# Optimization experiments

Hardware: AMD Instinct MI355X
Metric: run time of the kernel (lower is better)

Reference implementation:

```python
import jax, jax.numpy as jnp
import numpy as np

D, H, L, FF = 512, 8, 6, 2048
EPS = 1e-5


def _ln(x, g, b):
    m = x.mean(-1, keepdims=True)
    v = ((x - m) ** 2).mean(-1, keepdims=True)
    return (x - m) * jax.lax.rsqrt(v + EPS) * g + b


def _mha(qi, ki, vi, w, b):
    # w: [4, D, D] (q, k, v, out), b: [4, D]; weights stored [in, out]
    B, Sq, _ = qi.shape
    Sk = ki.shape[1]
    dk = D // H
    q = (qi @ w[0] + b[0]).reshape(B, Sq, H, dk)
    k = (ki @ w[1] + b[1]).reshape(B, Sk, H, dk)
    v = (vi @ w[2] + b[2]).reshape(B, Sk, H, dk)
    scores = jnp.einsum('bqhd,bkhd->bhqk', q, k) / np.float32(np.sqrt(dk))
    attn = jax.nn.softmax(scores, axis=-1)
    o = jnp.einsum('bhqk,bkhd->bqhd', attn, v).reshape(B, Sq, D)
    return o @ w[3] + b[3]


def setup_inputs() -> dict:
    key = jax.random.key(0)
    ks = jax.random.split(key, 12)
    bs, c, h, w = 4, D, 32, 32
    nq = 100
    s = np.float32(0.02)
    f32 = jnp.float32
    return {
        'src': jax.random.normal(ks[0], (bs, c, h, w), f32),
        'query_embed': jax.random.normal(ks[1], (nq, D), f32),
        'pos_embed': jax.random.normal(ks[2], (bs, c, h, w), f32),
        # encoder params (stacked over L layers)
        'enc_attn_w': jax.random.normal(ks[3], (L, 4, D, D), f32) * s,
        'enc_attn_b': jnp.zeros((L, 4, D), f32),
        'enc_w1': jax.random.normal(ks[4], (L, D, FF), f32) * s,
        'enc_b1': jnp.zeros((L, FF), f32),
        'enc_w2': jax.random.normal(ks[5], (L, FF, D), f32) * s,
        'enc_b2': jnp.zeros((L, D), f32),
        'enc_ln_w': jnp.ones((L, 2, D), f32),
        'enc_ln_b': jnp.zeros((L, 2, D), f32),
        # decoder params
        'dec_sa_w': jax.random.normal(ks[6], (L, 4, D, D), f32) * s,
        'dec_sa_b': jnp.zeros((L, 4, D), f32),
        'dec_ca_w': jax.random.normal(ks[7], (L, 4, D, D), f32) * s,
        'dec_ca_b': jnp.zeros((L, 4, D), f32),
        'dec_w1': jax.random.normal(ks[8], (L, D, FF), f32) * s,
        'dec_b1': jnp.zeros((L, FF), f32),
        'dec_w2': jax.random.normal(ks[9], (L, FF, D), f32) * s,
        'dec_b2': jnp.zeros((L, D), f32),
        'dec_ln_w': jnp.ones((L, 3, D), f32),
        'dec_ln_b': jnp.zeros((L, 3, D), f32),
    }


def reference(src, query_embed, pos_embed,
              enc_attn_w, enc_attn_b, enc_w1, enc_b1, enc_w2, enc_b2,
              enc_ln_w, enc_ln_b,
              dec_sa_w, dec_sa_b, dec_ca_w, dec_ca_b,
              dec_w1, dec_b1, dec_w2, dec_b2, dec_ln_w, dec_ln_b):
    bs, c, h, w = src.shape
    x = src.reshape(bs, c, h * w).transpose(0, 2, 1)        # [B, HW, D]
    pos = pos_embed.reshape(bs, c, h * w).transpose(0, 2, 1)  # [B, HW, D]
    qe = jnp.broadcast_to(query_embed[None], (bs,) + query_embed.shape)  # [B, NQ, D]

    def enc_step(mem, p):
        aw, ab, w1, b1, w2, b2, lnw, lnb = p
        t = mem + pos  # original re-adds pos_embed every encoder layer
        t = _ln(t + _mha(t, t, t, aw, ab), lnw[0], lnb[0])
        f = jax.nn.relu(t @ w1 + b1) @ w2 + b2
        t = _ln(t + f, lnw[1], lnb[1])
        return t, None

    memory, _ = jax.lax.scan(
        enc_step, x,
        (enc_attn_w, enc_attn_b, enc_w1, enc_b1, enc_w2, enc_b2, enc_ln_w, enc_ln_b))

    mem_in = memory + pos

    def dec_step(out, p):
        saw, sab, caw, cab, w1, b1, w2, b2, lnw, lnb = p
        t = out + qe  # original re-adds query_embed every decoder layer
        t = _ln(t + _mha(t, t, t, saw, sab), lnw[0], lnb[0])
        t = _ln(t + _mha(t, mem_in, mem_in, caw, cab), lnw[1], lnb[1])
        f = jax.nn.relu(t @ w1 + b1) @ w2 + b2
        t = _ln(t + f, lnw[2], lnb[2])
        return t, None

    tgt = jnp.zeros_like(qe)
    output, _ = jax.lax.scan(
        dec_step, tgt,
        (dec_sa_w, dec_sa_b, dec_ca_w, dec_ca_b, dec_w1, dec_b1, dec_w2, dec_b2,
         dec_ln_w, dec_ln_b))
    return output, memory
```

## Files before the change

kernel.cpp:

```cpp
#include <hip/hip_runtime.h>
#include <math.h>


typedef unsigned short bfu;
typedef unsigned int u32;
typedef __bf16 bf8v __attribute__((ext_vector_type(8)));
typedef float f32x4 __attribute__((ext_vector_type(4)));

__device__ inline bfu f2bf(float f) {
  union { float f; u32 u; } v; v.f = f;
  u32 u = v.u;
  u32 r = (u + 0x7fffu + ((u >> 16) & 1u)) >> 16;
  return (bfu)r;
}
__device__ inline float bflo(u32 u) { return __uint_as_float(u << 16); }

typedef const __attribute__((address_space(1))) u32 gas_t;
typedef __attribute__((address_space(3))) u32 las_t;
__device__ __forceinline__ void gl16(const void* g, void* l) {
  __builtin_amdgcn_global_load_lds((gas_t*)g, (las_t*)l, 16, 0, 0);
}

__global__ __launch_bounds__(256) void k_transpose(const float* __restrict__ in,
                                                   float* __restrict__ out) {
  __shared__ float tile[32][33];
  int b = blockIdx.z;
  int c0 = blockIdx.x * 32, s0 = blockIdx.y * 32;
  int tx = threadIdx.x, ty = threadIdx.y;
  for (int i = ty; i < 32; i += 8)
    tile[i][tx] = in[((size_t)(b * 512 + c0 + i)) * 1024 + s0 + tx];
  __syncthreads();
  for (int i = ty; i < 32; i += 8)
    out[((size_t)(b * 1024 + s0 + i)) * 512 + c0 + tx] = tile[tx][i];
}

__global__ __launch_bounds__(256) void k_wt(const float* __restrict__ src,
                                            bfu* __restrict__ dst,
                                            int K, int N, int nj, int lstride) {
  __shared__ bfu tile[32][33];
  int g = blockIdx.z;
  int l = g / nj, j = g - l * nj;
  const float* s = src + ((size_t)l * lstride + j) * (size_t)K * N;
  bfu* d = dst + (size_t)g * (size_t)K * N;
  int n0 = blockIdx.x * 32, k0 = blockIdx.y * 32;
  int tx = threadIdx.x, ty = threadIdx.y;
  for (int i = ty; i < 32; i += 8)
    tile[i][tx] = f2bf(s[(size_t)(k0 + i) * N + n0 + tx]);
  __syncthreads();
  for (int i = ty; i < 32; i += 8)
    d[(size_t)(n0 + i) * K + k0 + tx] = tile[tx][i];
}

__global__ void k_add_dual(const float* __restrict__ a, const float* __restrict__ b,
                           float* __restrict__ of, bfu* __restrict__ ob, int n4) {
  int i = blockIdx.x * blockDim.x + threadIdx.x;
  if (i >= n4) return;
  float4 x = ((const float4*)a)[i];
  float4 y = ((const float4*)b)[i];
  float4 r = make_float4(x.x + y.x, x.y + y.y, x.z + y.z, x.w + y.w);
  if (of) ((float4*)of)[i] = r;
  if (ob) ((ushort4*)ob)[i] = make_ushort4(f2bf(r.x), f2bf(r.y), f2bf(r.z), f2bf(r.w));
}

__global__ void k_add_qe_dual(const float* __restrict__ a, const float* __restrict__ qe,
                              float* __restrict__ of, bfu* __restrict__ ob) {
  int i = blockIdx.x * blockDim.x + threadIdx.x;
  if (i >= 51200) return;
  int row = i >> 7;
  int q = row % 100;
  int c4 = i & 127;
  float4 x = ((const float4*)a)[i];
  float4 y = ((const float4*)qe)[q * 128 + c4];
  float4 r = make_float4(x.x + y.x, x.y + y.y, x.z + y.z, x.w + y.w);
  if (of) ((float4*)of)[i] = r;
  if (ob) ((ushort4*)ob)[i] = make_ushort4(f2bf(r.x), f2bf(r.y), f2bf(r.z), f2bf(r.w));
}

__global__ void k_zero(float* __restrict__ o, int n4) {
  int i = blockIdx.x * blockDim.x + threadIdx.x;
  if (i < n4) ((float4*)o)[i] = make_float4(0.f, 0.f, 0.f, 0.f);
}

__global__ __launch_bounds__(256) void k_ln_red(const float* __restrict__ A,
                                                const float* __restrict__ P,
                                                int nsplit, size_t pz,
                                                const float* __restrict__ bias,
                                                const float* __restrict__ g,
                                                const float* __restrict__ be,
                                                float* __restrict__ of,
                                                bfu* __restrict__ ob, int rows) {
  int row = blockIdx.x * 4 + (threadIdx.x >> 6);
  int lane = threadIdx.x & 63;
  if (row >= rows) return;
  const float* pa = A + (size_t)row * 512;
  float v[8];
  float s = 0.f, s2 = 0.f;
#pragma unroll
  for (int j = 0; j < 8; ++j) {
    int c = lane + j * 64;
    float x = pa[c] + bias[c];
    for (int z = 0; z < nsplit; ++z) x += P[z * pz + (size_t)row * 512 + c];
    v[j] = x; s += x; s2 += x * x;
  }
#pragma unroll
  for (int off = 32; off > 0; off >>= 1) {
    s += __shfl_xor(s, off);
    s2 += __shfl_xor(s2, off);
  }
  float mean = s * (1.f / 512.f);
  float var = s2 * (1.f / 512.f) - mean * mean;
  float r = rsqrtf(var + 1e-5f);
#pragma unroll
  for (int j = 0; j < 8; ++j) {
    int c = lane + j * 64;
    float o = (v[j] - mean) * r * g[c] + be[c];
    of[(size_t)row * 512 + c] = o;
    if (ob) ob[(size_t)row * 512 + c] = f2bf(o);
  }
}

__global__ __launch_bounds__(256) void k_gemm_bf(const bfu* __restrict__ A,
                                                 const bfu* __restrict__ Wt,
                                                 const float* __restrict__ bias,
                                                 bfu* __restrict__ C,
                                                 int M, int N, int K, int relu,
                                                 size_t wtz, size_t cz, int bz) {
  __shared__ bfu As[2][128][64];
  __shared__ bfu Bs[2][128][64];
  int z = blockIdx.z;
  Wt += (size_t)z * wtz; C += (size_t)z * cz; bias += z * bz;
  int bm = blockIdx.y * 128, bn = blockIdx.x * 128;
  int t = threadIdx.x;
  int wave = t >> 6, lane = t & 63;
  int wm = wave >> 1, wn = wave & 1;
  int l15 = lane & 15, l4 = lane >> 4;
  f32x4 acc[4][4];
  f32x4 zz = {0.f, 0.f, 0.f, 0.f};
#pragma unroll
  for (int mi = 0; mi < 4; ++mi)
#pragma unroll
    for (int ni = 0; ni < 4; ++ni) acc[mi][ni] = zz;

  auto stage = [&](int buf, int k0) {
#pragma unroll
    for (int i = 0; i < 4; ++i) {
      int c = t + i * 256;
      int row = c >> 3, kg = c & 7;
      int sc = kg ^ (row & 7);
      if (bm + row < M)
        gl16(A + (size_t)(bm + row) * K + k0 + sc * 8, &As[buf][row][kg * 8]);
      gl16(Wt + (size_t)(bn + row) * K + k0 + sc * 8, &Bs[buf][row][kg * 8]);
    }
  };
  stage(0, 0);
  int cur = 0;
  for (int k0 = 0; k0 < K; k0 += 64) {
    __syncthreads();
    if (k0 + 64 < K) stage(cur ^ 1, k0 + 64);
#pragma unroll
    for (int kc = 0; kc < 2; ++kc) {
      bf8v av[4], bv[4];
#pragma unroll
      for (int mi = 0; mi < 4; ++mi) {
        int row = wm * 64 + mi * 16 + l15;
        av[mi] = *(const bf8v*)&As[cur][row][((kc * 4 + l4) ^ (row & 7)) * 8];
      }
#pragma unroll
      for (int ni = 0; ni < 4; ++ni) {
        int row = wn * 64 + ni * 16 + l15;
        bv[ni] = *(const bf8v*)&Bs[cur][row][((kc * 4 + l4) ^ (row & 7)) * 8];
      }
#pragma unroll
      for (int mi = 0; mi < 4; ++mi)
#pragma unroll
        for (int ni = 0; ni < 4; ++ni)
          acc[mi][ni] = __builtin_amdgcn_mfma_f32_16x16x32_bf16(av[mi], bv[ni],
                                                                acc[mi][ni], 0, 0, 0);
    }
    cur ^= 1;
  }

#pragma unroll
  for (int mi = 0; mi < 4; ++mi) {
    int row0 = bm + wm * 64 + mi * 16 + l4 * 4;
#pragma unroll
    for (int ni = 0; ni < 4; ++ni) {
      int col = bn + wn * 64 + ni * 16 + l15;
      float bb = bias[col];
#pragma unroll
      for (int r = 0; r < 4; ++r) {
        int row = row0 + r;
        if (row < M) {
          float v = acc[mi][ni][r] + bb;
          if (relu) v = fmaxf(v, 0.f);
          C[(size_t)row * N + col] = f2bf(v);
        }
      }
    }
  }
}

__global__ __launch_bounds__(256) void k_gemm_sk(const bfu* __restrict__ A,
                                                 const bfu* __restrict__ Wt,
                                                 float* __restrict__ Pf,
                                                 int M, int N, int K, int ksplit) {
  __shared__ bfu As[2][128][64];
  __shared__ bfu Bs[2][128][64];
  int z = blockIdx.z;
  int Kc = K / ksplit;
  int kbeg = z * Kc;
  Pf += (size_t)z * M * N;
  int bm = blockIdx.y * 128, bn = blockIdx.x * 128;
  int t = threadIdx.x;
  int wave = t >> 6, lane = t & 63;
  int wm = wave >> 1, wn = wave & 1;
  int l15 = lane & 15, l4 = lane >> 4;
  f32x4 acc[4][4];
  f32x4 zz = {0.f, 0.f, 0.f, 0.f};
#pragma unroll
  for (int mi = 0; mi < 4; ++mi)
#pragma unroll
    for (int ni = 0; ni < 4; ++ni) acc[mi][ni] = zz;

  auto stage = [&](int buf, int k0) {
#pragma unroll
    for (int i = 0; i < 4; ++i) {
      int c = t + i * 256;
      int row = c >> 3, kg = c & 7;
      int sc = kg ^ (row & 7);
      if (bm + row < M)
        gl16(A + (size_t)(bm + row) * K + k0 + sc * 8, &As[buf][row][kg * 8]);
      gl16(Wt + (size_t)(bn + row) * K + k0 + sc * 8, &Bs[buf][row][kg * 8]);
    }
  };
  stage(0, kbeg);
  int cur = 0;
  for (int k0 = kbeg; k0 < kbeg + Kc; k0 += 64) {
    __syncthreads();
    if (k0 + 64 < kbeg + Kc) stage(cur ^ 1, k0 + 64);
#pragma unroll
    for (int kc = 0; kc < 2; ++kc) {
      bf8v av[4], bv[4];
#pragma unroll
      for (int mi = 0; mi < 4; ++mi) {
        int row = wm * 64 + mi * 16 + l15;
        av[mi] = *(const bf8v*)&As[cur][row][((kc * 4 + l4) ^ (row & 7)) * 8];
      }
#pragma unroll
      for (int ni = 0; ni < 4; ++ni) {
        int row = wn * 64 + ni * 16 + l15;
        bv[ni] = *(const bf8v*)&Bs[cur][row][((kc * 4 + l4) ^ (row & 7)) * 8];
      }
#pragma unroll
      for (int mi = 0; mi < 4; ++mi)
#pragma unroll
        for (int ni = 0; ni < 4; ++ni)
          acc[mi][ni] = __builtin_amdgcn_mfma_f32_16x16x32_bf16(av[mi], bv[ni],
                                                                acc[mi][ni], 0, 0, 0);
    }
    cur ^= 1;
  }

#pragma unroll
  for (int mi = 0; mi < 4; ++mi) {
    int row0 = bm + wm * 64 + mi * 16 + l4 * 4;
#pragma unroll
    for (int ni = 0; ni < 4; ++ni) {
      int col = bn + wn * 64 + ni * 16 + l15;
#pragma unroll
      for (int r = 0; r < 4; ++r) {
        int row = row0 + r;
        if (row < M) Pf[(size_t)row * N + col] = acc[mi][ni][r];
      }
    }
  }
}

__global__ __launch_bounds__(256) void k_attn_mfma(const bfu* __restrict__ Q, int qs,
                                                   const bfu* __restrict__ Km,
                                                   const bfu* __restrict__ Vm, int kvs,
                                                   bfu* __restrict__ O,
                                                   int Sq, int Sk) {
  __shared__ bfu Ks[64][72];
  __shared__ bfu Vt[64][72];
  __shared__ bfu Sm[4][16][72];
  const float scale = 0.125f;
  int b = blockIdx.z, h = blockIdx.y;
  int q0 = blockIdx.x * 64;
  int t = threadIdx.x;
  int wave = t >> 6, lane = t & 63;
  int l15 = lane & 15, l4 = lane >> 4;
  int hoff = h * 64;

  uint4 uq0 = {0u, 0u, 0u, 0u}, uq1 = {0u, 0u, 0u, 0u};
  {
    int qrow = q0 + wave * 16 + l15;
    if (qrow < Sq) {
      const bfu* qp = Q + (size_t)(b * Sq + qrow) * qs + hoff + l4 * 8;
      uq0 = *(const uint4*)qp;
      uq1 = *(const uint4*)(qp + 32);
    }
  }
  bf8v qf0 = *(bf8v*)&uq0, qf1 = *(bf8v*)&uq1;

  float m_[4] = {-1e30f, -1e30f, -1e30f, -1e30f};
  float l_[4] = {0.f, 0.f, 0.f, 0.f};
  f32x4 oacc[4];
  f32x4 zz = {0.f, 0.f, 0.f, 0.f};
#pragma unroll
  for (int n = 0; n < 4; ++n) oacc[n] = zz;

  uint4 ruk[2], ruv[2];
  const uint4 uz = {0u, 0u, 0u, 0u};
  auto load_kv = [&](int k0) {
#pragma unroll
    for (int i = 0; i < 2; ++i) {
      int e = t + i * 256;
      int rk = e >> 3, cg = e & 7;
      ruk[i] = uz;
      if (k0 + rk < Sk)
        ruk[i] = *(const uint4*)(Km + (size_t)(b * Sk + k0 + rk) * kvs + hoff + cg * 8);
      int kv = e & 63, dg = e >> 6;
      ruv[i] = uz;
      if (k0 + kv < Sk)
        ruv[i] = *(const uint4*)(Vm + (size_t)(b * Sk + k0 + kv) * kvs + hoff + dg * 8);
    }
  };
  load_kv(0);

  for (int k0 = 0; k0 < Sk; k0 += 64) {
#pragma unroll
    for (int i = 0; i < 2; ++i) {
      int e = t + i * 256;
      int rk = e >> 3, cg = e & 7;
      *(uint4*)&Ks[rk][cg * 8] = ruk[i];
      int kv = e & 63, dg = e >> 6;
      bfu vv[8];
      *(uint4*)vv = ruv[i];
#pragma unroll
      for (int j = 0; j < 8; ++j) Vt[dg * 8 + j][kv] = vv[j];
    }
    __syncthreads();
    if (k0 + 64 < Sk) load_kv(k0 + 64);

    f32x4 s4[4];
#pragma unroll
    for (int tt = 0; tt < 4; ++tt) {
      bf8v kf0 = *(const bf8v*)&Ks[tt * 16 + l15][l4 * 8];
      bf8v kf1 = *(const bf8v*)&Ks[tt * 16 + l15][32 + l4 * 8];
      f32x4 a = zz;
      a = __builtin_amdgcn_mfma_f32_16x16x32_bf16(qf0, kf0, a, 0, 0, 0);
      a = __builtin_amdgcn_mfma_f32_16x16x32_bf16(qf1, kf1, a, 0, 0, 0);
      s4[tt] = a;
    }

    float f_[4];
#pragma unroll
    for (int r = 0; r < 4; ++r) {
      float sv[4];
      float mx = -1e30f;
#pragma unroll
      for (int tt = 0; tt < 4; ++tt) {
        float s = s4[tt][r] * scale;
        s = (k0 + tt * 16 + l15 < Sk) ? s : -1e30f;
        sv[tt] = s;
        mx = fmaxf(mx, s);
      }
#pragma unroll
      for (int off = 1; off < 16; off <<= 1) mx = fmaxf(mx, __shfl_xor(mx, off));
      float nm = fmaxf(m_[r], mx);
      float f = __expf(m_[r] - nm);
      float ps = 0.f;
#pragma unroll
      for (int tt = 0; tt < 4; ++tt) {
        float p = __expf(sv[tt] - nm);
        ps += p;
        Sm[wave][l4 * 4 + r][tt * 16 + l15] = f2bf(p);
      }
#pragma unroll
      for (int off = 1; off < 16; off <<= 1) ps += __shfl_xor(ps, off);
      l_[r] = l_[r] * f + ps;
      m_[r] = nm;
      f_[r] = f;
    }
#pragma unroll
    for (int n = 0; n < 4; ++n)
#pragma unroll
      for (int r = 0; r < 4; ++r) oacc[n][r] *= f_[r];

    bf8v p0 = *(const bf8v*)&Sm[wave][l15][l4 * 8];
    bf8v p1 = *(const bf8v*)&Sm[wave][l15][32 + l4 * 8];
#pragma unroll
    for (int n = 0; n < 4; ++n) {
      bf8v v0 = *(const bf8v*)&Vt[n * 16 + l15][l4 * 8];
      bf8v v1 = *(const bf8v*)&Vt[n * 16 + l15][32 + l4 * 8];
      oacc[n] = __builtin_amdgcn_mfma_f32_16x16x32_bf16(p0, v0, oacc[n], 0, 0, 0);
      oacc[n] = __builtin_amdgcn_mfma_f32_16x16x32_bf16(p1, v1, oacc[n], 0, 0, 0);
    }
    __syncthreads();
  }

#pragma unroll
  for (int r = 0; r < 4; ++r) {
    int row = q0 + wave * 16 + l4 * 4 + r;
    if (row < Sq) {
      float inv = 1.f / l_[r];
#pragma unroll
      for (int n = 0; n < 4; ++n)
        O[(size_t)(b * Sq + row) * 512 + hoff + n * 16 + l15] = f2bf(oacc[n][r] * inv);
    }
  }
}


extern "C" void kernel_launch(void* const* d_in, const int* in_sizes, int n_in,
                              void* d_out, int out_size, void* d_ws, size_t ws_size,
                              hipStream_t stream) {
  const float* src         = (const float*)d_in[0];
  const float* query_embed = (const float*)d_in[1];
  const float* pos_embed   = (const float*)d_in[2];
  const float* enc_attn_w  = (const float*)d_in[3];
  const float* enc_attn_b  = (const float*)d_in[4];
  const float* enc_w1      = (const float*)d_in[5];
  const float* enc_b1      = (const float*)d_in[6];
  const float* enc_w2      = (const float*)d_in[7];
  const float* enc_b2      = (const float*)d_in[8];
  const float* enc_ln_w    = (const float*)d_in[9];
  const float* enc_ln_b    = (const float*)d_in[10];
  const float* dec_sa_w    = (const float*)d_in[11];
  const float* dec_sa_b    = (const float*)d_in[12];
  const float* dec_ca_w    = (const float*)d_in[13];
  const float* dec_ca_b    = (const float*)d_in[14];
  const float* dec_w1      = (const float*)d_in[15];
  const float* dec_b1      = (const float*)d_in[16];
  const float* dec_w2      = (const float*)d_in[17];
  const float* dec_b2      = (const float*)d_in[18];
  const float* dec_ln_w    = (const float*)d_in[19];
  const float* dec_ln_b    = (const float*)d_in[20];
  float* out = (float*)d_out;

  const size_t ENC = 4UL * 1024 * 512;
  const size_t DEC = 4UL * 100 * 512;
  const size_t MAT = 512UL * 512;

  float* p = (float*)d_ws;
  float* x    = p; p += ENC;
  float* pos  = p; p += ENC;
  float* t1   = p; p += ENC;
  float* t2   = p; p += ENC;
  float* t3   = p; p += DEC;
  float* dstr = p; p += DEC;
  float* Pf   = p; p += 4 * ENC;

  bfu* bp = (bfu*)p;
  bfu* t1b    = bp; bp += ENC;
  bfu* t2b    = bp; bp += ENC;
  bfu* t3b    = bp; bp += DEC;
  bfu* qkvb   = bp; bp += 4096UL * 1536;
  bfu* aob    = bp; bp += ENC;
  bfu* mob    = bp; bp += ENC;
  bfu* hbb    = bp; bp += 4096UL * 2048;
  bfu* meminb = bp; bp += ENC;
  bfu* ckvb   = bp; bp += 6UL * 4096 * 1024;
  bfu* enc_qkv_t = bp; bp += 18 * MAT;
  bfu* enc_out_t = bp; bp += 6 * MAT;
  bfu* enc_w1t   = bp; bp += 6UL * 512 * 2048;
  bfu* enc_w2t   = bp; bp += 6UL * 2048 * 512;
  bfu* dsa_qkv_t = bp; bp += 18 * MAT;
  bfu* dsa_out_t = bp; bp += 6 * MAT;
  bfu* dca_q_t   = bp; bp += 6 * MAT;
  bfu* dca_kv_t  = bp; bp += 12 * MAT;
  bfu* dca_out_t = bp; bp += 6 * MAT;
  bfu* dw1t      = bp; bp += 6UL * 512 * 2048;
  bfu* dw2t      = bp; bp += 6UL * 2048 * 512;

  dim3 tb(32, 8);
  k_transpose<<<dim3(16, 32, 4), tb, 0, stream>>>(src, x);
  k_transpose<<<dim3(16, 32, 4), tb, 0, stream>>>(pos_embed, pos);

  k_wt<<<dim3(16, 16, 18), tb, 0, stream>>>(enc_attn_w,            enc_qkv_t, 512, 512, 3, 4);
  k_wt<<<dim3(16, 16, 6),  tb, 0, stream>>>(enc_attn_w + 3 * MAT,  enc_out_t, 512, 512, 1, 4);
  k_wt<<<dim3(64, 16, 6),  tb, 0, stream>>>(enc_w1,                enc_w1t,   512, 2048, 1, 1);
  k_wt<<<dim3(16, 64, 6),  tb, 0, stream>>>(enc_w2,                enc_w2t,   2048, 512, 1, 1);
  k_wt<<<dim3(16, 16, 18), tb, 0, stream>>>(dec_sa_w,              dsa_qkv_t, 512, 512, 3, 4);
  k_wt<<<dim3(16, 16, 6),  tb, 0, stream>>>(dec_sa_w + 3 * MAT,    dsa_out_t, 512, 512, 1, 4);
  k_wt<<<dim3(16, 16, 6),  tb, 0, stream>>>(dec_ca_w,              dca_q_t,   512, 512, 1, 4);
  k_wt<<<dim3(16, 16, 12), tb, 0, stream>>>(dec_ca_w + 1 * MAT,    dca_kv_t,  512, 512, 2, 4);
  k_wt<<<dim3(16, 16, 6),  tb, 0, stream>>>(dec_ca_w + 3 * MAT,    dca_out_t, 512, 512, 1, 4);
  k_wt<<<dim3(64, 16, 6),  tb, 0, stream>>>(dec_w1,                dw1t,      512, 2048, 1, 1);
  k_wt<<<dim3(16, 64, 6),  tb, 0, stream>>>(dec_w2,                dw2t,      2048, 512, 1, 1);

  for (int l = 0; l < 6; ++l) {
    const float* ab = enc_attn_b + (size_t)l * 2048;
    float* xout = (l == 5) ? (out + DEC) : x;
    k_add_dual<<<2048, 256, 0, stream>>>(x, pos, t1, t1b, (int)(ENC / 4));
    k_gemm_bf<<<dim3(12, 32), 256, 0, stream>>>(t1b, enc_qkv_t + (size_t)l * 3 * MAT, ab,
                                                qkvb, 4096, 1536, 512, 0, 0, 0, 0);
    k_attn_mfma<<<dim3(16, 8, 4), 256, 0, stream>>>(qkvb, 1536, qkvb + 512, qkvb + 1024, 1536,
                                                    aob, 1024, 1024);
    k_gemm_sk<<<dim3(4, 32, 2), 256, 0, stream>>>(aob, enc_out_t + (size_t)l * MAT, Pf,
                                                  4096, 512, 512, 2);
    k_ln_red<<<1024, 256, 0, stream>>>(t1, Pf, 2, ENC, ab + 1536,
                                       enc_ln_w + (size_t)(l * 2 + 0) * 512,
                                       enc_ln_b + (size_t)(l * 2 + 0) * 512, t2, t2b, 4096);
    k_gemm_bf<<<dim3(16, 32), 256, 0, stream>>>(t2b, enc_w1t + (size_t)l * 512 * 2048,
                                                enc_b1 + (size_t)l * 2048, hbb,
                                                4096, 2048, 512, 1, 0, 0, 0);
    k_gemm_sk<<<dim3(4, 32, 4), 256, 0, stream>>>(hbb, enc_w2t + (size_t)l * 2048 * 512, Pf,
                                                  4096, 512, 2048, 4);
    k_ln_red<<<1024, 256, 0, stream>>>(t2, Pf, 4, ENC, enc_b2 + (size_t)l * 512,
                                       enc_ln_w + (size_t)(l * 2 + 1) * 512,
                                       enc_ln_b + (size_t)(l * 2 + 1) * 512,
                                       xout, (bfu*)nullptr, 4096);
  }

  k_add_dual<<<2048, 256, 0, stream>>>(out + DEC, pos, (float*)nullptr, meminb, (int)(ENC / 4));
  k_zero<<<200, 256, 0, stream>>>(dstr, (int)(DEC / 4));

  k_gemm_bf<<<dim3(8, 32, 6), 256, 0, stream>>>(meminb, dca_kv_t, dec_ca_b + 512,
                                                ckvb, 4096, 1024, 512, 0,
                                                2 * MAT, 4096UL * 1024, 2048);

  for (int l = 0; l < 6; ++l) {
    const float* sb = dec_sa_b + (size_t)l * 2048;
    const float* cb = dec_ca_b + (size_t)l * 2048;
    float* dout = (l == 5) ? out : dstr;
    k_add_qe_dual<<<200, 256, 0, stream>>>(dstr, query_embed, t1, t1b);
    k_gemm_bf<<<dim3(12, 4), 256, 0, stream>>>(t1b, dsa_qkv_t + (size_t)l * 3 * MAT, sb,
                                               qkvb, 400, 1536, 512, 0, 0, 0, 0);
    k_attn_mfma<<<dim3(2, 8, 4), 256, 0, stream>>>(qkvb, 1536, qkvb + 512, qkvb + 1024, 1536,
                                                   aob, 100, 100);
    k_gemm_sk<<<dim3(4, 4, 2), 256, 0, stream>>>(aob, dsa_out_t + (size_t)l * MAT, Pf,
                                                 400, 512, 512, 2);
    k_ln_red<<<100, 256, 0, stream>>>(t1, Pf, 2, 400UL * 512, sb + 1536,
                                      dec_ln_w + (size_t)(l * 3 + 0) * 512,
                                      dec_ln_b + (size_t)(l * 3 + 0) * 512, t2, t2b, 400);
    k_gemm_bf<<<dim3(4, 4), 256, 0, stream>>>(t2b, dca_q_t + (size_t)l * MAT, cb,
                                              qkvb, 400, 512, 512, 0, 0, 0, 0);
    k_attn_mfma<<<dim3(2, 8, 4), 256, 0, stream>>>(qkvb, 512,
                                                   ckvb + (size_t)l * 4096 * 1024,
                                                   ckvb + (size_t)l * 4096 * 1024 + 512, 1024,
                                                   aob, 100, 1024);
    k_gemm_sk<<<dim3(4, 4, 2), 256, 0, stream>>>(aob, dca_out_t + (size_t)l * MAT, Pf,
                                                 400, 512, 512, 2);
    k_ln_red<<<100, 256, 0, stream>>>(t2, Pf, 2, 400UL * 512, cb + 1536,
                                      dec_ln_w + (size_t)(l * 3 + 1) * 512,
                                      dec_ln_b + (size_t)(l * 3 + 1) * 512, t3, t3b, 400);
    k_gemm_bf<<<dim3(16, 4), 256, 0, stream>>>(t3b, dw1t + (size_t)l * 512 * 2048,
                                               dec_b1 + (size_t)l * 2048, hbb,
                                               400, 2048, 512, 1, 0, 0, 0);
    k_gemm_sk<<<dim3(4, 4, 4), 256, 0, stream>>>(hbb, dw2t + (size_t)l * 2048 * 512, Pf,
                                                 400, 512, 2048, 4);
    k_ln_red<<<100, 256, 0, stream>>>(t3, Pf, 4, 400UL * 512, dec_b2 + (size_t)l * 512,
                                      dec_ln_w + (size_t)(l * 3 + 2) * 512,
                                      dec_ln_b + (size_t)(l * 3 + 2) * 512,
                                      dout, (bfu*)nullptr, 400);
  }
}
```

Baseline: 2.034 ms.

## Fuse positional/query embedding adds into LayerNorm epilogue and widen attention KV tiles

The final LayerNorm of each encoder/decoder layer now also adds pos_embed (or query_embed) and writes the next layer's fp32 and bf16 inputs. This removes the separate add kernels, the zeroing kernel and the extra tensor round-trips. The attention kernel also processes 128 keys per tile instead of 64 and raises wave priority around the MFMA sections, halving loop iterations and barriers. The cost is more LDS and registers per block, which may reduce occupancy.

```diff
diff --git a/kernel.cpp b/kernel.cpp
--- a/kernel.cpp
+++ b/kernel.cpp
@@ -58,27 +58,20 @@
   float4 x = ((const float4*)a)[i];
   float4 y = ((const float4*)b)[i];
   float4 r = make_float4(x.x + y.x, x.y + y.y, x.z + y.z, x.w + y.w);
-  if (of) ((float4*)of)[i] = r;
-  if (ob) ((ushort4*)ob)[i] = make_ushort4(f2bf(r.x), f2bf(r.y), f2bf(r.z), f2bf(r.w));
-}
-
-__global__ void k_add_qe_dual(const float* __restrict__ a, const float* __restrict__ qe,
-                              float* __restrict__ of, bfu* __restrict__ ob) {
+  ((float4*)of)[i] = r;
+  ((ushort4*)ob)[i] = make_ushort4(f2bf(r.x), f2bf(r.y), f2bf(r.z), f2bf(r.w));
+}
+
+__global__ void k_qe0(const float* __restrict__ qe, float* __restrict__ of,
+                      bfu* __restrict__ ob) {
   int i = blockIdx.x * blockDim.x + threadIdx.x;
   if (i >= 51200) return;
   int row = i >> 7;
   int q = row % 100;
   int c4 = i & 127;
-  float4 x = ((const float4*)a)[i];
   float4 y = ((const float4*)qe)[q * 128 + c4];
-  float4 r = make_float4(x.x + y.x, x.y + y.y, x.z + y.z, x.w + y.w);
-  if (of) ((float4*)of)[i] = r;
-  if (ob) ((ushort4*)ob)[i] = make_ushort4(f2bf(r.x), f2bf(r.y), f2bf(r.z), f2bf(r.w));
-}
-
-__global__ void k_zero(float* __restrict__ o, int n4) {
-  int i = blockIdx.x * blockDim.x + threadIdx.x;
-  if (i < n4) ((float4*)o)[i] = make_float4(0.f, 0.f, 0.f, 0.f);
+  ((float4*)of)[i] = y;
+  ((ushort4*)ob)[i] = make_ushort4(f2bf(y.x), f2bf(y.y), f2bf(y.z), f2bf(y.w));
 }
 
 __global__ __launch_bounds__(256) void k_ln_red(const float* __restrict__ A,
@@ -88,7 +81,12 @@
                                                 const float* __restrict__ g,
                                                 const float* __restrict__ be,
                                                 float* __restrict__ of,
-                                                bfu* __restrict__ ob, int rows) {
+                                                bfu* __restrict__ ob,
+                                                const float* __restrict__ add2,
+                                                int qe_mode,
+                                                float* __restrict__ of2,
+                                                bfu* __restrict__ ob2,
+                                                int rows) {
   int row = blockIdx.x * 4 + (threadIdx.x >> 6);
   int lane = threadIdx.x & 63;
   if (row >= rows) return;
@@ -110,12 +108,18 @@
   float mean = s * (1.f / 512.f);
   float var = s2 * (1.f / 512.f) - mean * mean;
   float r = rsqrtf(var + 1e-5f);
+  int arow = qe_mode ? (row % 100) : row;
 #pragma unroll
   for (int j = 0; j < 8; ++j) {
     int c = lane + j * 64;
     float o = (v[j] - mean) * r * g[c] + be[c];
-    of[(size_t)row * 512 + c] = o;
+    if (of) of[(size_t)row * 512 + c] = o;
     if (ob) ob[(size_t)row * 512 + c] = f2bf(o);
+    if (add2) {
+      float o2 = o + add2[(size_t)arow * 512 + c];
+      if (of2) of2[(size_t)row * 512 + c] = o2;
+      if (ob2) ob2[(size_t)row * 512 + c] = f2bf(o2);
+    }
   }
 }
 
@@ -281,9 +285,9 @@
                                                    const bfu* __restrict__ Vm, int kvs,
                                                    bfu* __restrict__ O,
                                                    int Sq, int Sk) {
-  __shared__ bfu Ks[64][72];
-  __shared__ bfu Vt[64][72];
-  __shared__ bfu Sm[4][16][72];
+  __shared__ bfu Ks[128][72];
+  __shared__ bfu Vt[64][136];
+  __shared__ bfu Sm[4][16][136];
   const float scale = 0.125f;
   int b = blockIdx.z, h = blockIdx.y;
   int q0 = blockIdx.x * 64;
@@ -310,17 +314,17 @@
 #pragma unroll
   for (int n = 0; n < 4; ++n) oacc[n] = zz;
 
-  uint4 ruk[2], ruv[2];
+  uint4 ruk[4], ruv[4];
   const uint4 uz = {0u, 0u, 0u, 0u};
   auto load_kv = [&](int k0) {
 #pragma unroll
-    for (int i = 0; i < 2; ++i) {
+    for (int i = 0; i < 4; ++i) {
       int e = t + i * 256;
       int rk = e >> 3, cg = e & 7;
       ruk[i] = uz;
       if (k0 + rk < Sk)
         ruk[i] = *(const uint4*)(Km + (size_t)(b * Sk + k0 + rk) * kvs + hoff + cg * 8);
-      int kv = e & 63, dg = e >> 6;
+      int kv = e & 127, dg = e >> 7;
       ruv[i] = uz;
       if (k0 + kv < Sk)
         ruv[i] = *(const uint4*)(Vm + (size_t)(b * Sk + k0 + kv) * kvs + hoff + dg * 8);
@@ -328,24 +332,25 @@
   };
   load_kv(0);
 
-  for (int k0 = 0; k0 < Sk; k0 += 64) {
-#pragma unroll
-    for (int i = 0; i < 2; ++i) {
+  for (int k0 = 0; k0 < Sk; k0 += 128) {
+#pragma unroll
+    for (int i = 0; i < 4; ++i) {
       int e = t + i * 256;
       int rk = e >> 3, cg = e & 7;
       *(uint4*)&Ks[rk][cg * 8] = ruk[i];
-      int kv = e & 63, dg = e >> 6;
+      int kv = e & 127, dg = e >> 7;
       bfu vv[8];
       *(uint4*)vv = ruv[i];
 #pragma unroll
       for (int j = 0; j < 8; ++j) Vt[dg * 8 + j][kv] = vv[j];
     }
     __syncthreads();
-    if (k0 + 64 < Sk) load_kv(k0 + 64);
-
-    f32x4 s4[4];
-#pragma unroll
-    for (int tt = 0; tt < 4; ++tt) {
+    if (k0 + 128 < Sk) load_kv(k0 + 128);
+
+    f32x4 s4[8];
+    __builtin_amdgcn_s_setprio(1);
+#pragma unroll
+    for (int tt = 0; tt < 8; ++tt) {
       bf8v kf0 = *(const bf8v*)&Ks[tt * 16 + l15][l4 * 8];
       bf8v kf1 = *(const bf8v*)&Ks[tt * 16 + l15][32 + l4 * 8];
       f32x4 a = zz;
@@ -353,14 +358,15 @@
       a = __builtin_amdgcn_mfma_f32_16x16x32_bf16(qf1, kf1, a, 0, 0, 0);
       s4[tt] = a;
     }
+    __builtin_amdgcn_s_setprio(0);
 
     float f_[4];
 #pragma unroll
     for (int r = 0; r < 4; ++r) {
-      float sv[4];
+      float sv[8];
       float mx = -1e30f;
 #pragma unroll
-      for (int tt = 0; tt < 4; ++tt) {
+      for (int tt = 0; tt < 8; ++tt) {
         float s = s4[tt][r] * scale;
         s = (k0 + tt * 16 + l15 < Sk) ? s : -1e30f;
         sv[tt] = s;
@@ -372,7 +378,7 @@
       float f = __expf(m_[r] - nm);
       float ps = 0.f;
 #pragma unroll
-      for (int tt = 0; tt < 4; ++tt) {
+      for (int tt = 0; tt < 8; ++tt) {
         float p = __expf(sv[tt] - nm);
         ps += p;
         Sm[wave][l4 * 4 + r][tt * 16 + l15] = f2bf(p);
@@ -388,15 +394,20 @@
 #pragma unroll
       for (int r = 0; r < 4; ++r) oacc[n][r] *= f_[r];
 
-    bf8v p0 = *(const bf8v*)&Sm[wave][l15][l4 * 8];
-    bf8v p1 = *(const bf8v*)&Sm[wave][l15][32 + l4 * 8];
-#pragma unroll
-    for (int n = 0; n < 4; ++n) {
-      bf8v v0 = *(const bf8v*)&Vt[n * 16 + l15][l4 * 8];
-      bf8v v1 = *(const bf8v*)&Vt[n * 16 + l15][32 + l4 * 8];
-      oacc[n] = __builtin_amdgcn_mfma_f32_16x16x32_bf16(p0, v0, oacc[n], 0, 0, 0);
-      oacc[n] = __builtin_amdgcn_mfma_f32_16x16x32_bf16(p1, v1, oacc[n], 0, 0, 0);
-    }
+    __builtin_amdgcn_s_setprio(1);
+#pragma unroll
+    for (int h2 = 0; h2 < 2; ++h2) {
+      bf8v p0 = *(const bf8v*)&Sm[wave][l15][h2 * 64 + l4 * 8];
+      bf8v p1 = *(const bf8v*)&Sm[wave][l15][h2 * 64 + 32 + l4 * 8];
+#pragma unroll
+      for (int n = 0; n < 4; ++n) {
+        bf8v v0 = *(const bf8v*)&Vt[n * 16 + l15][h2 * 64 + l4 * 8];
+        bf8v v1 = *(const bf8v*)&Vt[n * 16 + l15][h2 * 64 + 32 + l4 * 8];
+        oacc[n] = __builtin_amdgcn_mfma_f32_16x16x32_bf16(p0, v0, oacc[n], 0, 0, 0);
+        oacc[n] = __builtin_amdgcn_mfma_f32_16x16x32_bf16(p1, v1, oacc[n], 0, 0, 0);
+      }
+    }
+    __builtin_amdgcn_s_setprio(0);
     __syncthreads();
   }
 
@@ -449,7 +460,6 @@
   float* t1   = p; p += ENC;
   float* t2   = p; p += ENC;
   float* t3   = p; p += DEC;
-  float* dstr = p; p += DEC;
   float* Pf   = p; p += 4 * ENC;
 
   bfu* bp = (bfu*)p;
@@ -458,7 +468,6 @@
   bfu* t3b    = bp; bp += DEC;
   bfu* qkvb   = bp; bp += 4096UL * 1536;
   bfu* aob    = bp; bp += ENC;
-  bfu* mob    = bp; bp += ENC;
   bfu* hbb    = bp; bp += 4096UL * 2048;
   bfu* meminb = bp; bp += ENC;
   bfu* ckvb   = bp; bp += 6UL * 4096 * 1024;
@@ -490,10 +499,9 @@
   k_wt<<<dim3(64, 16, 6),  tb, 0, stream>>>(dec_w1,                dw1t,      512, 2048, 1, 1);
   k_wt<<<dim3(16, 64, 6),  tb, 0, stream>>>(dec_w2,                dw2t,      2048, 512, 1, 1);
 
+  k_add_dual<<<2048, 256, 0, stream>>>(x, pos, t1, t1b, (int)(ENC / 4));
   for (int l = 0; l < 6; ++l) {
     const float* ab = enc_attn_b + (size_t)l * 2048;
-    float* xout = (l == 5) ? (out + DEC) : x;
-    k_add_dual<<<2048, 256, 0, stream>>>(x, pos, t1, t1b, (int)(ENC / 4));
     k_gemm_bf<<<dim3(12, 32), 256, 0, stream>>>(t1b, enc_qkv_t + (size_t)l * 3 * MAT, ab,
                                                 qkvb, 4096, 1536, 512, 0, 0, 0, 0);
     k_attn_mfma<<<dim3(16, 8, 4), 256, 0, stream>>>(qkvb, 1536, qkvb + 512, qkvb + 1024, 1536,
@@ -502,30 +510,37 @@
                                                   4096, 512, 512, 2);
     k_ln_red<<<1024, 256, 0, stream>>>(t1, Pf, 2, ENC, ab + 1536,
                                        enc_ln_w + (size_t)(l * 2 + 0) * 512,
-                                       enc_ln_b + (size_t)(l * 2 + 0) * 512, t2, t2b, 4096);
+                                       enc_ln_b + (size_t)(l * 2 + 0) * 512,
+                                       t2, t2b, (const float*)nullptr, 0,
+                                       (float*)nullptr, (bfu*)nullptr, 4096);
     k_gemm_bf<<<dim3(16, 32), 256, 0, stream>>>(t2b, enc_w1t + (size_t)l * 512 * 2048,
                                                 enc_b1 + (size_t)l * 2048, hbb,
                                                 4096, 2048, 512, 1, 0, 0, 0);
     k_gemm_sk<<<dim3(4, 32, 4), 256, 0, stream>>>(hbb, enc_w2t + (size_t)l * 2048 * 512, Pf,
                                                   4096, 512, 2048, 4);
-    k_ln_red<<<1024, 256, 0, stream>>>(t2, Pf, 4, ENC, enc_b2 + (size_t)l * 512,
-                                       enc_ln_w + (size_t)(l * 2 + 1) * 512,
-                                       enc_ln_b + (size_t)(l * 2 + 1) * 512,
-                                       xout, (bfu*)nullptr, 4096);
-  }
-
-  k_add_dual<<<2048, 256, 0, stream>>>(out + DEC, pos, (float*)nullptr, meminb, (int)(ENC / 4));
-  k_zero<<<200, 256, 0, stream>>>(dstr, (int)(DEC / 4));
+    if (l < 5) {
+      k_ln_red<<<1024, 256, 0, stream>>>(t2, Pf, 4, ENC, enc_b2 + (size_t)l * 512,
+                                         enc_ln_w + (size_t)(l * 2 + 1) * 512,
+                                         enc_ln_b + (size_t)(l * 2 + 1) * 512,
+                                         (float*)nullptr, (bfu*)nullptr,
+                                         pos, 0, t1, t1b, 4096);
+    } else {
+      k_ln_red<<<1024, 256, 0, stream>>>(t2, Pf, 4, ENC, enc_b2 + (size_t)l * 512,
+                                         enc_ln_w + (size_t)(l * 2 + 1) * 512,
+                                         enc_ln_b + (size_t)(l * 2 + 1) * 512,
+                                         out + DEC, (bfu*)nullptr,
+                                         pos, 0, (float*)nullptr, meminb, 4096);
+    }
+  }
 
   k_gemm_bf<<<dim3(8, 32, 6), 256, 0, stream>>>(meminb, dca_kv_t, dec_ca_b + 512,
                                                 ckvb, 4096, 1024, 512, 0,
                                                 2 * MAT, 4096UL * 1024, 2048);
 
+  k_qe0<<<200, 256, 0, stream>>>(query_embed, t1, t1b);
   for (int l = 0; l < 6; ++l) {
     const float* sb = dec_sa_b + (size_t)l * 2048;
     const float* cb = dec_ca_b + (size_t)l * 2048;
-    float* dout = (l == 5) ? out : dstr;
-    k_add_qe_dual<<<200, 256, 0, stream>>>(dstr, query_embed, t1, t1b);
     k_gemm_bf<<<dim3(12, 4), 256, 0, stream>>>(t1b, dsa_qkv_t + (size_t)l * 3 * MAT, sb,
                                                qkvb, 400, 1536, 512, 0, 0, 0, 0);
     k_attn_mfma<<<dim3(2, 8, 4), 256, 0, stream>>>(qkvb, 1536, qkvb + 512, qkvb + 1024, 1536,
@@ -534,7 +549,9 @@
                                                  400, 512, 512, 2);
     k_ln_red<<<100, 256, 0, stream>>>(t1, Pf, 2, 400UL * 512, sb + 1536,
                                       dec_ln_w + (size_t)(l * 3 + 0) * 512,
-                                      dec_ln_b + (size_t)(l * 3 + 0) * 512, t2, t2b, 400);
+                                      dec_ln_b + (size_t)(l * 3 + 0) * 512,
+                                      t2, t2b, (const float*)nullptr, 0,
+                                      (float*)nullptr, (bfu*)nullptr, 400);
     k_gemm_bf<<<dim3(4, 4), 256, 0, stream>>>(t2b, dca_q_t + (size_t)l * MAT, cb,
                                               qkvb, 400, 512, 512, 0, 0, 0, 0);
     k_attn_mfma<<<dim3(2, 8, 4), 256, 0, stream>>>(qkvb, 512,
@@ -545,15 +562,27 @@
                                                  400, 512, 512, 2);
     k_ln_red<<<100, 256, 0, stream>>>(t2, Pf, 2, 400UL * 512, cb + 1536,
                                       dec_ln_w + (size_t)(l * 3 + 1) * 512,
-                                      dec_ln_b + (size_t)(l * 3 + 1) * 512, t3, t3b, 400);
+                                      dec_ln_b + (size_t)(l * 3 + 1) * 512,
+                                      t3, t3b, (const float*)nullptr, 0,
+                                      (float*)nullptr, (bfu*)nullptr, 400);
     k_gemm_bf<<<dim3(16, 4), 256, 0, stream>>>(t3b, dw1t + (size_t)l * 512 * 2048,
                                                dec_b1 + (size_t)l * 2048, hbb,
                                                400, 2048, 512, 1, 0, 0, 0);
     k_gemm_sk<<<dim3(4, 4, 4), 256, 0, stream>>>(hbb, dw2t + (size_t)l * 2048 * 512, Pf,
                                                  400, 512, 2048, 4);
-    k_ln_red<<<100, 256, 0, stream>>>(t3, Pf, 4, 400UL * 512, dec_b2 + (size_t)l * 512,
-                                      dec_ln_w + (size_t)(l * 3 + 2) * 512,
-                                      dec_ln_b + (size_t)(l * 3 + 2) * 512,
-                                      dout, (bfu*)nullptr, 400);
-  }
-}
+    if (l < 5) {
+      k_ln_red<<<100, 256, 0, stream>>>(t3, Pf, 4, 400UL * 512, dec_b2 + (size_t)l * 512,
+                                        dec_ln_w + (size_t)(l * 3 + 2) * 512,
+                                        dec_ln_b + (size_t)(l * 3 + 2) * 512,
+                                        (float*)nullptr, (bfu*)nullptr,
+                                        query_embed, 1, t1, t1b, 400);
+    } else {
+      k_ln_red<<<100, 256, 0, stream>>>(t3, Pf, 4, 400UL * 512, dec_b2 + (size_t)l * 512,
+                                        dec_ln_w + (size_t)(l * 3 + 2) * 512,
+                                        dec_ln_b + (size_t)(l * 3 + 2) * 512,
+                                        out, (bfu*)nullptr,
+                                        (const float*)nullptr, 0,
+                                        (float*)nullptr, (bfu*)nullptr, 400);
+    }
+  }
+}
```

Result: no change. 1.997 ms (-1.8%).
